# Performance work log

Measured on AMD Instinct MI355X. Metric: run time of the kernel, lower is better.

Reference implementation:

```python
import jax, jax.numpy as jnp
import numpy as np

B, L, H, NH, P = 4, 1024, 1024, 16, 2048
HD = H // NH


def setup_inputs() -> dict:
    key = jax.random.key(0)
    ks = jax.random.split(key, 6)
    x = jax.random.normal(ks[0], (B, L, H), dtype=jnp.float32)
    # torch.nn.Linear weights are [out, in]
    Wqkv = jax.random.normal(ks[1], (3 * H, H), dtype=jnp.float32) * 0.02
    bqkv = jnp.zeros((3 * H,), dtype=jnp.float32)
    Wo = jax.random.normal(ks[2], (H, H), dtype=jnp.float32) * 0.02
    bo = jnp.zeros((H,), dtype=jnp.float32)
    Er = jax.random.normal(ks[3], (NH, P, HD), dtype=jnp.float32)
    # causal mask: True where attention is disallowed (masked_fill semantics)
    mask = jnp.triu(jnp.ones((L, L), dtype=bool), k=1)
    return {"x": x, "mask": mask, "Wqkv": Wqkv, "bqkv": bqkv,
            "Wo": Wo, "bo": bo, "Er": Er}


def reference(x, mask, Wqkv, bqkv, Wo, bo, Er):
    b, l, d = x.shape
    nh, p, hd = Er.shape
    qkv = x @ Wqkv.T + bqkv                      # [b, l, 3d]
    q, k, v = jnp.split(qkv, 3, axis=-1)
    q = q.reshape(b, l, nh, hd).transpose(0, 2, 1, 3)   # [b, nh, l, hd]
    k = k.reshape(b, l, nh, hd).transpose(0, 2, 1, 3)
    v = v.reshape(b, l, nh, hd).transpose(0, 2, 1, 3)

    scores = jnp.einsum('bnlh,bnkh->bnlk', q, k) / jnp.sqrt(
        jnp.asarray(hd, dtype=x.dtype))

    # relative positions (j - i), torch negative-index wraparound -> mod p
    pos = jnp.arange(l)
    rel = (pos[None, :] - pos[:, None]) % p      # [l, l] in [0, p)
    # Equivalent to einsum('bnlh,rnlkh->bnlk', q, Er[:, rel][None]) but
    # computed as q @ Er^T over all positions then gathered (same math,
    # avoids materializing the [nh, l, l, hd] tensor).
    QEr_full = jnp.einsum('bnlh,nph->bnlp', q, Er)       # [b, nh, l, p]
    i_idx = pos[:, None]                          # broadcasts with rel
    QEr = QEr_full[:, :, i_idx, rel]              # [b, nh, l, l]

    a = scores + QEr
    a = jnp.where(mask, -jnp.inf, a)
    a = jax.nn.softmax(a, axis=-1)                # dropout: eval mode (identity)

    out = jnp.einsum('bnlk,bnkh->bnlh', a, v)     # [b, nh, l, hd]
    out = out.transpose(0, 2, 1, 3).reshape(b, l, d)
    return out @ Wo.T + bo
```

## Files before the change

### kernel.cpp

```cpp
#include <hip/hip_runtime.h>

typedef unsigned short u16;
typedef __bf16 bf16x8 __attribute__((ext_vector_type(8)));
typedef unsigned short u16x8 __attribute__((ext_vector_type(8)));
typedef unsigned short u16x4 __attribute__((ext_vector_type(4)));
typedef float f32x4 __attribute__((ext_vector_type(4)));

#define MFMA16(a, b, c) __builtin_amdgcn_mfma_f32_16x16x32_bf16((a), (b), (c), 0, 0, 0)

#define WAVE_LDS_FENCE() do { \
  asm volatile("s_waitcnt lgkmcnt(0)" ::: "memory"); \
  __builtin_amdgcn_sched_barrier(0); \
} while (0)

#define PIPE_WAIT(N) do { \
  asm volatile("s_waitcnt vmcnt(" #N ")" ::: "memory"); \
  __builtin_amdgcn_sched_barrier(0); \
  __builtin_amdgcn_s_barrier(); \
  __builtin_amdgcn_sched_barrier(0); \
} while (0)

#define GLDS(gp, lp) __builtin_amdgcn_global_load_lds( \
    (const __attribute__((address_space(1))) unsigned int*)(gp), \
    (__attribute__((address_space(3))) unsigned int*)(lp), 16, 0, 0)

__device__ __forceinline__ u16 f2b(float f) {
  unsigned u = __float_as_uint(f);
  u += 0x7fffu + ((u >> 16) & 1u);
  return (u16)(u >> 16);
}
__device__ __forceinline__ float b2f(u16 h) {
  return __uint_as_float(((unsigned)h) << 16);
}

__global__ void cvt_all(const float* __restrict__ x, u16* __restrict__ xb,
                        const float* __restrict__ w1, u16* __restrict__ w1b,
                        const float* __restrict__ w2, u16* __restrict__ w2b) {
  int i = blockIdx.x * blockDim.x + threadIdx.x;
  const float* s; u16* d; int off;
  if (i < 1048576)      { s = x;  d = xb;  off = i; }
  else if (i < 1835008) { s = w1; d = w1b; off = i - 1048576; }
  else                  { s = w2; d = w2b; off = i - 1835008; }
  float4 v = *(const float4*)(s + (size_t)off * 4);
  *(ushort4*)(d + (size_t)off * 4) = make_ushort4(f2b(v.x), f2b(v.y), f2b(v.z), f2b(v.w));
}

__global__ void build_F(const float* __restrict__ Er, u16* __restrict__ Fb) {
  int i = blockIdx.x * blockDim.x + threadIdx.x;
  int base = i * 4;
  int d = base & 63;
  int m = (base >> 6) & 1023;
  int n = base >> 16;
  int sm = (2048 - m) & 2047;
  float4 v = *(const float4*)(Er + ((size_t)(n * 2048 + sm) * 64 + d));
  *(ushort4*)(Fb + (size_t)base) = make_ushort4(f2b(v.x), f2b(v.y), f2b(v.z), f2b(v.w));
}

__global__ __launch_bounds__(256) void gemm_qkv(const u16* __restrict__ A, const u16* __restrict__ Bw,
                                                const float* __restrict__ bias,
                                                u16* __restrict__ Qo, u16* __restrict__ Ko,
                                                u16* __restrict__ Vt) {
  __shared__ u16 As[3][4][128][8];
  __shared__ u16 Bs[3][4][128][8];
  const int orig = blockIdx.y * 24 + blockIdx.x;
  const int xcd = orig & 7, q = orig >> 3;
  const int mt = ((xcd >> 1) << 3) + q / 12;
  const int nt = (xcd & 1) * 12 + q % 12;
  const int m0 = mt * 128, n0 = nt * 128;
  const int t = threadIdx.x, lane = t & 63, w = t >> 6;
  const int wr = w >> 1, wc = w & 1;
  const int l16 = lane & 15, lg = lane >> 4;
  f32x4 acc[4][4] = {};
  const int r0 = t & 127, g0 = t >> 7;
  const int g1 = g0 + 2;

#define STAGE(buf, k0) do { \
    GLDS(&A[(size_t)(m0 + r0) * 1024 + (k0) + g0 * 8], &As[buf][g0][r0][0]); \
    GLDS(&A[(size_t)(m0 + r0) * 1024 + (k0) + g1 * 8], &As[buf][g1][r0][0]); \
    GLDS(&Bw[(size_t)(n0 + r0) * 1024 + (k0) + g0 * 8], &Bs[buf][g0][r0][0]); \
    GLDS(&Bw[(size_t)(n0 + r0) * 1024 + (k0) + g1 * 8], &Bs[buf][g1][r0][0]); \
  } while (0)

  STAGE(0, 0);
  STAGE(1, 32);

  int buf = 0;
  for (int kt = 0; kt < 32; ++kt) {
    if (kt < 31) PIPE_WAIT(4); else PIPE_WAIT(0);
    if (kt < 30) {
      int nb = buf + 2; if (nb >= 3) nb -= 3;
      STAGE(nb, (kt + 2) * 32);
      __builtin_amdgcn_sched_barrier(0);
    }
    bf16x8 af[4], bfr[4];
#pragma unroll
    for (int m = 0; m < 4; ++m) af[m] = *(const bf16x8*)&As[buf][lg][wr * 64 + m * 16 + l16][0];
#pragma unroll
    for (int n = 0; n < 4; ++n) bfr[n] = *(const bf16x8*)&Bs[buf][lg][wc * 64 + n * 16 + l16][0];
#pragma unroll
    for (int m = 0; m < 4; ++m)
#pragma unroll
      for (int n = 0; n < 4; ++n) acc[m][n] = MFMA16(af[m], bfr[n], acc[m][n]);
    if (++buf == 3) buf = 0;
  }
#undef STAGE

#pragma unroll
  for (int n = 0; n < 4; ++n) {
    int col = n0 + wc * 64 + n * 16 + l16;
    float bq = bias[col];
    int which = col >> 10;
    int h = col & 1023;
    int head = h >> 6, d = h & 63;
    if (which == 2) {
#pragma unroll
      for (int m = 0; m < 4; ++m) {
        int row = m0 + wr * 64 + m * 16 + lg * 4;
        int b = row >> 10, ii = row & 1023;
        u16x4 o;
#pragma unroll
        for (int r = 0; r < 4; ++r) o[r] = f2b(acc[m][n][r] + bq);
        *(u16x4*)&Vt[(size_t)(((b * 16 + head) << 6) + d) * 1024 + ii] = o;
      }
    } else {
      u16* dst = which == 0 ? Qo : Ko;
      float scale = which == 1 ? 0.125f : 1.0f;
#pragma unroll
      for (int m = 0; m < 4; ++m) {
#pragma unroll
        for (int r = 0; r < 4; ++r) {
          int row = m0 + wr * 64 + m * 16 + lg * 4 + r;
          int b = row >> 10, ii = row & 1023;
          dst[(size_t)(((b * 16 + head) << 10) + ii) * 64 + d] = f2b((acc[m][n][r] + bq) * scale);
        }
      }
    }
  }
}

__global__ __launch_bounds__(256) void gemm_out(const u16* __restrict__ A, const u16* __restrict__ Bw,
                                                const float* __restrict__ bias, float* __restrict__ Co) {
  __shared__ u16 As[3][4][128][8];
  __shared__ u16 Bs[3][4][128][8];
  const int orig = blockIdx.y * 8 + blockIdx.x;
  const int xcd = orig & 7, q = orig >> 3;
  const int mt = (xcd << 2) + (q >> 3);
  const int nt = q & 7;
  const int m0 = mt * 128, n0 = nt * 128;
  const int t = threadIdx.x, lane = t & 63, w = t >> 6;
  const int wr = w >> 1, wc = w & 1;
  const int l16 = lane & 15, lg = lane >> 4;
  f32x4 acc[4][4] = {};
  const int r0 = t & 127, g0 = t >> 7;
  const int g1 = g0 + 2;

#define STAGE(buf, k0) do { \
    GLDS(&A[(size_t)(m0 + r0) * 1024 + (k0) + g0 * 8], &As[buf][g0][r0][0]); \
    GLDS(&A[(size_t)(m0 + r0) * 1024 + (k0) + g1 * 8], &As[buf][g1][r0][0]); \
    GLDS(&Bw[(size_t)(n0 + r0) * 1024 + (k0) + g0 * 8], &Bs[buf][g0][r0][0]); \
    GLDS(&Bw[(size_t)(n0 + r0) * 1024 + (k0) + g1 * 8], &Bs[buf][g1][r0][0]); \
  } while (0)

  STAGE(0, 0);
  STAGE(1, 32);

  int buf = 0;
  for (int kt = 0; kt < 32; ++kt) {
    if (kt < 31) PIPE_WAIT(4); else PIPE_WAIT(0);
    if (kt < 30) {
      int nb = buf + 2; if (nb >= 3) nb -= 3;
      STAGE(nb, (kt + 2) * 32);
      __builtin_amdgcn_sched_barrier(0);
    }
    bf16x8 af[4], bfr[4];
#pragma unroll
    for (int m = 0; m < 4; ++m) af[m] = *(const bf16x8*)&As[buf][lg][wr * 64 + m * 16 + l16][0];
#pragma unroll
    for (int n = 0; n < 4; ++n) bfr[n] = *(const bf16x8*)&Bs[buf][lg][wc * 64 + n * 16 + l16][0];
#pragma unroll
    for (int m = 0; m < 4; ++m)
#pragma unroll
      for (int n = 0; n < 4; ++n) acc[m][n] = MFMA16(af[m], bfr[n], acc[m][n]);
    if (++buf == 3) buf = 0;
  }
#undef STAGE

#pragma unroll
  for (int n = 0; n < 4; ++n) {
    int col = n0 + wc * 64 + n * 16 + l16;
    float bq = bias[col];
#pragma unroll
    for (int m = 0; m < 4; ++m) {
#pragma unroll
      for (int r = 0; r < 4; ++r) {
        int row = m0 + wr * 64 + m * 16 + lg * 4 + r;
        Co[(size_t)row * 1024 + col] = acc[m][n][r] + bq;
      }
    }
  }
}

__global__ __launch_bounds__(256) void attn_kernel(const u16* __restrict__ Qg, const u16* __restrict__ Kg,
                                                   const u16* __restrict__ Vtg, const u16* __restrict__ Fg,
                                                   u16* __restrict__ AO) {
  __shared__ u16 Kl[4096];
  __shared__ u16 Vl[4096];
  __shared__ u16 Fl[8192];
  __shared__ u16 BP[4][1024];

  const int bn = blockIdx.x;
  const int b = bn >> 4, n = bn & 15;
  const int qt = 15 - (int)blockIdx.y;
  const int i0 = qt * 64;
  const int t = threadIdx.x, lane = t & 63, w = t >> 6;
  const int l16 = lane & 15, lg = lane >> 4;

  const int rr0 = t >> 3, cc0 = t & 7;
  const int rr1 = (t + 256) >> 3, cc1 = t & 7;

  bf16x8 qf[2];
  {
    const u16* qp = &Qg[(size_t)((bn << 10) + i0 + (w << 4) + l16) * 64 + lg * 8];
    qf[0] = *(const bf16x8*)qp;
    qf[1] = *(const bf16x8*)(qp + 32);
  }

  {
    int mb0 = i0 - 63;
    int h0 = 64 + rr0, h1 = 64 + rr1;
    int gm0 = mb0 + h0; gm0 = gm0 < 0 ? 0 : (gm0 > 1023 ? 1023 : gm0);
    int gm1 = mb0 + h1; gm1 = gm1 < 0 ? 0 : (gm1 > 1023 ? 1023 : gm1);
    u16x8 a = *(const u16x8*)&Fg[(size_t)((n << 10) + gm0) * 64 + cc0 * 8];
    u16x8 c = *(const u16x8*)&Fg[(size_t)((n << 10) + gm1) * 64 + cc1 * 8];
    *(u16x8*)&Fl[h0 * 64 + (((cc0 ^ (h0 & 7)) & 7) << 3)] = a;
    *(u16x8*)&Fl[h1 * 64 + (((cc1 ^ (h1 & 7)) & 7) << 3)] = c;
  }

  float mrun[4], lsum[4];
  f32x4 ao[4] = {};
#pragma unroll
  for (int r = 0; r < 4; ++r) { mrun[r] = -3.0e38f; lsum[r] = 0.0f; }

  u16x8 rk0, rk1, rv0, rv1, rf0, rf1;

#define LOAD_STAGE(jt_) do { \
    int j0_ = (jt_) * 64, mb_ = i0 - j0_ - 63; \
    rk0 = *(const u16x8*)&Kg[(size_t)((bn << 10) + j0_ + rr0) * 64 + cc0 * 8]; \
    rk1 = *(const u16x8*)&Kg[(size_t)((bn << 10) + j0_ + rr1) * 64 + cc1 * 8]; \
    rv0 = *(const u16x8*)&Vtg[(size_t)((bn << 6) + rr0) * 1024 + j0_ + cc0 * 8]; \
    rv1 = *(const u16x8*)&Vtg[(size_t)((bn << 6) + rr1) * 1024 + j0_ + cc1 * 8]; \
    int m0_ = mb_ + rr0; m0_ = m0_ < 0 ? 0 : (m0_ > 1023 ? 1023 : m0_); \
    int m1_ = mb_ + rr1; m1_ = m1_ < 0 ? 0 : (m1_ > 1023 ? 1023 : m1_); \
    rf0 = *(const u16x8*)&Fg[(size_t)((n << 10) + m0_) * 64 + cc0 * 8]; \
    rf1 = *(const u16x8*)&Fg[(size_t)((n << 10) + m1_) * 64 + cc1 * 8]; \
  } while (0)

  LOAD_STAGE(0);

  for (int jt = 0; jt <= qt; ++jt) {
    const bool diag = (jt == qt);
    const int ph = (jt & 1) << 6;

    *(u16x8*)&Kl[rr0 * 64 + (((cc0 ^ (rr0 & 7)) & 7) << 3)] = rk0;
    *(u16x8*)&Kl[rr1 * 64 + (((cc1 ^ (rr1 & 7)) & 7) << 3)] = rk1;
    *(u16x8*)&Vl[rr0 * 64 + (((cc0 ^ (rr0 & 7)) & 7) << 3)] = rv0;
    *(u16x8*)&Vl[rr1 * 64 + (((cc1 ^ (rr1 & 7)) & 7) << 3)] = rv1;
    *(u16x8*)&Fl[(rr0 ^ ph) * 64 + (((cc0 ^ (rr0 & 7)) & 7) << 3)] = rf0;
    *(u16x8*)&Fl[(rr1 ^ ph) * 64 + (((cc1 ^ (rr1 & 7)) & 7) << 3)] = rf1;
    __syncthreads();

    if (jt < qt) LOAD_STAGE(jt + 1);

    __builtin_amdgcn_s_setprio(1);
    f32x4 sc[4] = {};
#pragma unroll
    for (int kk = 0; kk < 2; ++kk)
#pragma unroll
      for (int nn = 0; nn < 4; ++nn) {
        int jr = nn * 16 + l16;
        bf16x8 kb = *(const bf16x8*)&Kl[jr * 64 + ((((lg + 4 * kk) ^ (jr & 7)) & 7) << 3)];
        sc[nn] = MFMA16(qf[kk], kb, sc[nn]);
      }
    f32x4 bb[5] = {};
#pragma unroll
    for (int kk = 0; kk < 2; ++kk)
#pragma unroll
      for (int ct = 0; ct < 5; ++ct) {
        int trow = (w << 4) + ct * 16 + l16;
        bf16x8 fb = *(const bf16x8*)&Fl[(trow ^ ph) * 64 + ((((lg + 4 * kk) ^ (trow & 7)) & 7) << 3)];
        bb[ct] = MFMA16(qf[kk], fb, bb[ct]);
      }
    __builtin_amdgcn_s_setprio(0);

#pragma unroll
    for (int ct = 0; ct < 5; ++ct)
#pragma unroll
      for (int r = 0; r < 4; ++r) {
        int il = lg * 4 + r;
        int jl = il + 63 - (ct * 16 + l16);
        if ((unsigned)jl < 64u)
          BP[w][il * 64 + ((jl & 15) << 2) + (jl >> 4)] = f2b(bb[ct][r]);
      }
    WAVE_LDS_FENCE();

    float pv[4][4];
    float lmax[4];
#pragma unroll
    for (int r = 0; r < 4; ++r) {
      int il = lg * 4 + r;
      u16x4 gv = *(const u16x4*)&BP[w][il * 64 + (l16 << 2)];
      float m4 = -3.0e38f;
#pragma unroll
      for (int nn = 0; nn < 4; ++nn) {
        int jl = nn * 16 + l16;
        float s = sc[nn][r] + b2f(gv[nn]);
        if (diag && jl > (w << 4) + il) s = -1.0e30f;
        pv[nn][r] = s;
        m4 = fmaxf(m4, s);
      }
      lmax[r] = m4;
    }
    bool ok = (lmax[0] <= mrun[0] + 8.0f) && (lmax[1] <= mrun[1] + 8.0f) &&
              (lmax[2] <= mrun[2] + 8.0f) && (lmax[3] <= mrun[3] + 8.0f);
    if (__all(ok)) {
#pragma unroll
      for (int r = 0; r < 4; ++r) {
        float rs = 0.0f;
#pragma unroll
        for (int nn = 0; nn < 4; ++nn) {
          pv[nn][r] = __expf(pv[nn][r] - mrun[r]);
          rs += pv[nn][r];
        }
        lsum[r] += rs;
      }
    } else {
#pragma unroll
      for (int r = 0; r < 4; ++r) {
        float mx = lmax[r];
#pragma unroll
        for (int off = 1; off < 16; off <<= 1) mx = fmaxf(mx, __shfl_xor(mx, off));
        float mnew = fmaxf(mrun[r], mx);
        float scl = __expf(mrun[r] - mnew);
        float rs = 0.0f;
#pragma unroll
        for (int nn = 0; nn < 4; ++nn) {
          pv[nn][r] = __expf(pv[nn][r] - mnew);
          rs += pv[nn][r];
        }
        lsum[r] = lsum[r] * scl + rs;
        mrun[r] = mnew;
#pragma unroll
        for (int nd = 0; nd < 4; ++nd) ao[nd][r] *= scl;
      }
    }

#pragma unroll
    for (int nn = 0; nn < 4; ++nn)
#pragma unroll
      for (int r = 0; r < 4; ++r) {
        int i = lg * 4 + r, j = nn * 16 + l16;
        BP[w][i * 64 + ((((j >> 3) ^ (i & 7)) & 7) << 3) + (j & 7)] = f2b(pv[nn][r]);
      }
    WAVE_LDS_FENCE();
    __builtin_amdgcn_s_setprio(1);
#pragma unroll
    for (int kk = 0; kk < 2; ++kk) {
      bf16x8 pa = *(const bf16x8*)&BP[w][l16 * 64 + ((((lg + 4 * kk) ^ (l16 & 7)) & 7) << 3)];
#pragma unroll
      for (int nd = 0; nd < 4; ++nd) {
        int dr = nd * 16 + l16;
        bf16x8 vb = *(const bf16x8*)&Vl[dr * 64 + ((((lg + 4 * kk) ^ (dr & 7)) & 7) << 3)];
        ao[nd] = MFMA16(pa, vb, ao[nd]);
      }
    }
    __builtin_amdgcn_s_setprio(0);
    __syncthreads();
  }

#pragma unroll
  for (int r = 0; r < 4; ++r)
#pragma unroll
    for (int off = 1; off < 16; off <<= 1) lsum[r] += __shfl_xor(lsum[r], off);

#pragma unroll
  for (int nd = 0; nd < 4; ++nd)
#pragma unroll
    for (int r = 0; r < 4; ++r) {
      int i = i0 + (w << 4) + lg * 4 + r;
      int d = nd * 16 + l16;
      float v = ao[nd][r] / lsum[r];
      AO[(size_t)((b << 10) + i) * 1024 + n * 64 + d] = f2b(v);
    }
#undef LOAD_STAGE
}

extern "C" void kernel_launch(void* const* d_in, const int* in_sizes, int n_in,
                              void* d_out, int out_size, void* d_ws, size_t ws_size,
                              hipStream_t stream) {
  (void)in_sizes; (void)n_in; (void)out_size; (void)ws_size;
  const float* x    = (const float*)d_in[0];
  const float* Wqkv = (const float*)d_in[2];
  const float* bqkv = (const float*)d_in[3];
  const float* Wo   = (const float*)d_in[4];
  const float* bo   = (const float*)d_in[5];
  const float* Er   = (const float*)d_in[6];
  float* out = (float*)d_out;

  char* p = (char*)d_ws;
  u16* xb    = (u16*)p; p += (size_t)4096 * 1024 * 2;
  u16* wqkvb = (u16*)p; p += (size_t)3072 * 1024 * 2;
  u16* wob   = (u16*)p; p += (size_t)1024 * 1024 * 2;
  u16* Fb    = (u16*)p; p += (size_t)16 * 1024 * 64 * 2;
  u16* Qb    = (u16*)p; p += (size_t)64 * 1024 * 64 * 2;
  u16* Kb    = (u16*)p; p += (size_t)64 * 1024 * 64 * 2;
  u16* Vtb   = (u16*)p; p += (size_t)64 * 1024 * 64 * 2;
  u16* AO    = (u16*)p; p += (size_t)4096 * 1024 * 2;

  cvt_all<<<8192, 256, 0, stream>>>(x, xb, Wqkv, wqkvb, Wo, wob);
  build_F<<<1024, 256, 0, stream>>>(Er, Fb);
  gemm_qkv<<<dim3(24, 32), 256, 0, stream>>>(xb, wqkvb, bqkv, Qb, Kb, Vtb);
  attn_kernel<<<dim3(64, 16), 256, 0, stream>>>(Qb, Kb, Vtb, Fb, AO);
  gemm_out<<<dim3(8, 32), 256, 0, stream>>>(AO, wob, bo, out);
}
```

Before: 148.3 us.

## Enlarge QKV GEMM tiles to 256x256 with 512 threads and double buffering

After: 154.9 us. 4.4% more time.

```diff
diff --git a/kernel.cpp b/kernel.cpp
--- a/kernel.cpp
+++ b/kernel.cpp
@@ -56,52 +56,58 @@
   *(ushort4*)(Fb + (size_t)base) = make_ushort4(f2b(v.x), f2b(v.y), f2b(v.z), f2b(v.w));
 }
 
-__global__ __launch_bounds__(256) void gemm_qkv(const u16* __restrict__ A, const u16* __restrict__ Bw,
-                                                const float* __restrict__ bias,
-                                                u16* __restrict__ Qo, u16* __restrict__ Ko,
-                                                u16* __restrict__ Vt) {
-  __shared__ u16 As[3][4][128][8];
-  __shared__ u16 Bs[3][4][128][8];
-  const int orig = blockIdx.y * 24 + blockIdx.x;
+__global__ __launch_bounds__(512, 2) void gemm_qkv(const u16* __restrict__ A, const u16* __restrict__ Bw,
+                                                   const float* __restrict__ bias,
+                                                   u16* __restrict__ Qo, u16* __restrict__ Ko,
+                                                   u16* __restrict__ Vt) {
+  __shared__ u16 As[2][8][256][8];
+  __shared__ u16 Bs[2][8][256][8];
+  const int orig = blockIdx.y * 12 + blockIdx.x;
   const int xcd = orig & 7, q = orig >> 3;
-  const int mt = ((xcd >> 1) << 3) + q / 12;
-  const int nt = (xcd & 1) * 12 + q % 12;
-  const int m0 = mt * 128, n0 = nt * 128;
+  const int mt = ((xcd >> 1) << 2) + q / 6;
+  const int nt = (xcd & 1) * 6 + q % 6;
+  const int m0 = mt * 256, n0 = nt * 256;
   const int t = threadIdx.x, lane = t & 63, w = t >> 6;
-  const int wr = w >> 1, wc = w & 1;
+  const int wr = w >> 2, wc = w & 3;
   const int l16 = lane & 15, lg = lane >> 4;
-  f32x4 acc[4][4] = {};
-  const int r0 = t & 127, g0 = t >> 7;
-  const int g1 = g0 + 2;
-
-#define STAGE(buf, k0) do { \
-    GLDS(&A[(size_t)(m0 + r0) * 1024 + (k0) + g0 * 8], &As[buf][g0][r0][0]); \
-    GLDS(&A[(size_t)(m0 + r0) * 1024 + (k0) + g1 * 8], &As[buf][g1][r0][0]); \
-    GLDS(&Bw[(size_t)(n0 + r0) * 1024 + (k0) + g0 * 8], &Bs[buf][g0][r0][0]); \
-    GLDS(&Bw[(size_t)(n0 + r0) * 1024 + (k0) + g1 * 8], &Bs[buf][g1][r0][0]); \
+  f32x4 acc[8][4] = {};
+  const int sr = t & 255, sk = t >> 8;
+
+#define STAGE(bf, k0) do { \
+    GLDS(&A[(size_t)(m0 + sr) * 1024 + (k0) + (sk    ) * 8], &As[bf][sk    ][sr][0]); \
+    GLDS(&A[(size_t)(m0 + sr) * 1024 + (k0) + (sk + 2) * 8], &As[bf][sk + 2][sr][0]); \
+    GLDS(&A[(size_t)(m0 + sr) * 1024 + (k0) + (sk + 4) * 8], &As[bf][sk + 4][sr][0]); \
+    GLDS(&A[(size_t)(m0 + sr) * 1024 + (k0) + (sk + 6) * 8], &As[bf][sk + 6][sr][0]); \
+    GLDS(&Bw[(size_t)(n0 + sr) * 1024 + (k0) + (sk    ) * 8], &Bs[bf][sk    ][sr][0]); \
+    GLDS(&Bw[(size_t)(n0 + sr) * 1024 + (k0) + (sk + 2) * 8], &Bs[bf][sk + 2][sr][0]); \
+    GLDS(&Bw[(size_t)(n0 + sr) * 1024 + (k0) + (sk + 4) * 8], &Bs[bf][sk + 4][sr][0]); \
+    GLDS(&Bw[(size_t)(n0 + sr) * 1024 + (k0) + (sk + 6) * 8], &Bs[bf][sk + 6][sr][0]); \
   } while (0)
 
   STAGE(0, 0);
-  STAGE(1, 32);
+  PIPE_WAIT(0);
 
   int buf = 0;
-  for (int kt = 0; kt < 32; ++kt) {
-    if (kt < 31) PIPE_WAIT(4); else PIPE_WAIT(0);
-    if (kt < 30) {
-      int nb = buf + 2; if (nb >= 3) nb -= 3;
-      STAGE(nb, (kt + 2) * 32);
+  for (int kt = 0; kt < 16; ++kt) {
+    if (kt < 15) {
+      STAGE(buf ^ 1, (kt + 1) * 64);
       __builtin_amdgcn_sched_barrier(0);
     }
-    bf16x8 af[4], bfr[4];
-#pragma unroll
-    for (int m = 0; m < 4; ++m) af[m] = *(const bf16x8*)&As[buf][lg][wr * 64 + m * 16 + l16][0];
-#pragma unroll
-    for (int n = 0; n < 4; ++n) bfr[n] = *(const bf16x8*)&Bs[buf][lg][wc * 64 + n * 16 + l16][0];
-#pragma unroll
-    for (int m = 0; m < 4; ++m)
-#pragma unroll
-      for (int n = 0; n < 4; ++n) acc[m][n] = MFMA16(af[m], bfr[n], acc[m][n]);
-    if (++buf == 3) buf = 0;
+#pragma unroll
+    for (int kk = 0; kk < 2; ++kk) {
+      bf16x8 bfr[4];
+#pragma unroll
+      for (int n = 0; n < 4; ++n)
+        bfr[n] = *(const bf16x8*)&Bs[buf][lg + 4 * kk][wc * 64 + n * 16 + l16][0];
+#pragma unroll
+      for (int m = 0; m < 8; ++m) {
+        bf16x8 af = *(const bf16x8*)&As[buf][lg + 4 * kk][wr * 128 + m * 16 + l16][0];
+#pragma unroll
+        for (int n = 0; n < 4; ++n) acc[m][n] = MFMA16(af, bfr[n], acc[m][n]);
+      }
+    }
+    if (kt < 15) PIPE_WAIT(0);
+    buf ^= 1;
   }
 #undef STAGE
 
@@ -114,8 +120,8 @@
     int head = h >> 6, d = h & 63;
     if (which == 2) {
 #pragma unroll
-      for (int m = 0; m < 4; ++m) {
-        int row = m0 + wr * 64 + m * 16 + lg * 4;
+      for (int m = 0; m < 8; ++m) {
+        int row = m0 + wr * 128 + m * 16 + lg * 4;
         int b = row >> 10, ii = row & 1023;
         u16x4 o;
 #pragma unroll
@@ -126,10 +132,10 @@
       u16* dst = which == 0 ? Qo : Ko;
       float scale = which == 1 ? 0.125f : 1.0f;
 #pragma unroll
-      for (int m = 0; m < 4; ++m) {
+      for (int m = 0; m < 8; ++m) {
 #pragma unroll
         for (int r = 0; r < 4; ++r) {
-          int row = m0 + wr * 64 + m * 16 + lg * 4 + r;
+          int row = m0 + wr * 128 + m * 16 + lg * 4 + r;
           int b = row >> 10, ii = row & 1023;
           dst[(size_t)(((b * 16 + head) << 10) + ii) * 64 + d] = f2b((acc[m][n][r] + bq) * scale);
         }
@@ -418,7 +424,7 @@
 
   cvt_all<<<8192, 256, 0, stream>>>(x, xb, Wqkv, wqkvb, Wo, wob);
   build_F<<<1024, 256, 0, stream>>>(Er, Fb);
-  gemm_qkv<<<dim3(24, 32), 256, 0, stream>>>(xb, wqkvb, bqkv, Qb, Kb, Vtb);
+  gemm_qkv<<<dim3(12, 16), 512, 0, stream>>>(xb, wqkvb, bqkv, Qb, Kb, Vtb);
   attn_kernel<<<dim3(64, 16), 256, 0, stream>>>(Qb, Kb, Vtb, Fb, AO);
   gemm_out<<<dim3(8, 32), 256, 0, stream>>>(AO, wob, bo, out);
 }
```
